# Performance work log

Hardware: AMD Instinct MI355X
Metric: run time of the kernel (lower is better)

## Reference

```python
import jax, jax.numpy as jnp
import numpy as np

N, E = 50000, 800000
IN_CH, OUT_CH, HEADS = 128, 64, 4
NEG_SLOPE = 0.2
BN_EPS = 1e-5


def setup_inputs() -> dict:
    key = jax.random.key(0)
    ks = jax.random.split(key, 8)
    x = jax.random.normal(ks[0], (N, IN_CH), dtype=jnp.float32)
    edge_index = jax.random.randint(ks[1], (2, E), 0, N, dtype=jnp.int64)
    # GATConv params (concat=False: W projects to H*C, output averaged over heads)
    W = jax.random.normal(ks[2], (IN_CH, HEADS * OUT_CH), dtype=jnp.float32) * (1.0 / np.sqrt(IN_CH))
    att_src = jax.random.normal(ks[3], (HEADS, OUT_CH), dtype=jnp.float32) * 0.1
    att_dst = jax.random.normal(ks[4], (HEADS, OUT_CH), dtype=jnp.float32) * 0.1
    bias = jnp.zeros((OUT_CH,), dtype=jnp.float32)
    bn_weight = jnp.ones((OUT_CH,), dtype=jnp.float32)
    bn_bias = jnp.zeros((OUT_CH,), dtype=jnp.float32)
    return {"x": x, "edge_index": edge_index, "W": W, "att_src": att_src,
            "att_dst": att_dst, "bias": bias, "bn_weight": bn_weight, "bn_bias": bn_bias}


def reference(x, edge_index, W, att_src, att_dst, bias, bn_weight, bn_bias):
    # dropout p=0.3 on input and attention weights: identity in eval mode
    n = x.shape[0]
    x_proj = (x @ W).reshape(n, HEADS, OUT_CH)              # [N, H, C]
    a_src = jnp.einsum('nhc,hc->nh', x_proj, att_src)       # [N, H]
    a_dst = jnp.einsum('nhc,hc->nh', x_proj, att_dst)       # [N, H]

    # PyG default add_self_loops=True
    loops = jnp.arange(n, dtype=edge_index.dtype)
    src = jnp.concatenate([edge_index[0], loops])           # [E+N]
    dst = jnp.concatenate([edge_index[1], loops])           # [E+N]

    e = jax.nn.leaky_relu(a_src[src] + a_dst[dst], NEG_SLOPE)  # [E+N, H]
    # edge-softmax per destination node (numerically stable)
    m = jax.ops.segment_max(e, dst, num_segments=n)         # [N, H]
    ex = jnp.exp(e - m[dst])
    denom = jax.ops.segment_sum(ex, dst, num_segments=n)    # [N, H]
    alpha = ex / denom[dst]                                 # [E+N, H]

    msg = alpha[:, :, None] * x_proj[src]                   # [E+N, H, C]
    out = jax.ops.segment_sum(msg, dst, num_segments=n)     # [N, H, C]
    out = out.mean(axis=1) + bias                           # concat=False -> head mean

    # BatchNorm (training-mode batch statistics, biased variance)
    mu = out.mean(axis=0)
    var = out.var(axis=0)
    out = (out - mu) * jax.lax.rsqrt(var + BN_EPS) * bn_weight + bn_bias
    return jax.nn.elu(out)
```

## Files before the change

kernel.cpp:

```cpp
#include <hip/hip_runtime.h>

#define IN_CH 128
#define HC 256
#define OUT_CH 64
#define NEG 0.2f
#define BN_EPS 1e-5f
#define APITCH 136
#define CSR_CAP 8192

typedef __attribute__((ext_vector_type(8))) short short8v;
typedef __attribute__((ext_vector_type(4))) float f32x4v;

__device__ __forceinline__ float4 add4(float4 a, float4 b) {
    return make_float4(a.x + b.x, a.y + b.y, a.z + b.z, a.w + b.w);
}
__device__ __forceinline__ float4 mul4(float4 a, float4 b) {
    return make_float4(a.x * b.x, a.y * b.y, a.z * b.z, a.w * b.w);
}
__device__ __forceinline__ float4 exp4f(float4 a) {
    return make_float4(__expf(a.x), __expf(a.y), __expf(a.z), __expf(a.w));
}
__device__ __forceinline__ float4 leaky4(float4 v) {
    v.x = v.x > 0.f ? v.x : v.x * NEG;
    v.y = v.y > 0.f ? v.y : v.y * NEG;
    v.z = v.z > 0.f ? v.z : v.z * NEG;
    v.w = v.w > 0.f ? v.w : v.w * NEG;
    return v;
}
__device__ __forceinline__ unsigned short f2bf(float f) {
    unsigned u = __float_as_uint(f);
    unsigned r = u + 0x7fffu + ((u >> 16) & 1u);
    return (unsigned short)(r >> 16);
}
__device__ __forceinline__ void acc8(float4& a, float ws, unsigned u) {
    a.x += ws * (float)(u & 0xffu);
    a.y += ws * (float)((u >> 8) & 0xffu);
    a.z += ws * (float)((u >> 16) & 0xffu);
    a.w += ws * (float)(u >> 24);
}

__global__ __launch_bounds__(256) void prep_wt(const float* __restrict__ W,
                                               unsigned short* __restrict__ wt,
                                               unsigned* __restrict__ zeros, int nz) {
    int idx = blockIdx.x * 256 + threadIdx.x;
    if (idx < nz) zeros[idx] = 0u;
    if (idx >= 64 * 64) return;
    int frag = idx >> 6, l = idx & 63;
    int j = frag >> 2, ks = frag & 3;
    int c = l & 15, g = l >> 4;
    int ch = c * 16 + j;
    int k0 = ks * 32 + g * 8;
    unsigned up[4];
    #pragma unroll
    for (int q = 0; q < 4; ++q) {
        unsigned short lo = f2bf(W[(size_t)(k0 + 2 * q) * HC + ch]);
        unsigned short hi = f2bf(W[(size_t)(k0 + 2 * q + 1) * HC + ch]);
        up[q] = (unsigned)lo | ((unsigned)hi << 16);
    }
    *(uint4*)(wt + (size_t)idx * 8) = make_uint4(up[0], up[1], up[2], up[3]);
}

__global__ __launch_bounds__(256) void gemm_mfma(const float* __restrict__ x,
                                                 const unsigned short* __restrict__ wt,
                                                 const float* __restrict__ att_src,
                                                 const float* __restrict__ att_dst,
                                                 unsigned char* __restrict__ xq,
                                                 float* __restrict__ pks,
                                                 float* __restrict__ adst, int N) {
    __shared__ unsigned short Al[64][APITCH];
    int t = threadIdx.x;
    int r0 = blockIdx.x * 64;
    #pragma unroll
    for (int i = 0; i < 8; ++i) {
        int f4 = t + i * 256;
        int m = f4 >> 5, kf = f4 & 31;
        float4 v = make_float4(0.f, 0.f, 0.f, 0.f);
        int r = r0 + m;
        if (r < N) v = *(const float4*)(x + (size_t)r * IN_CH + kf * 4);
        ushort4 pk;
        pk.x = f2bf(v.x); pk.y = f2bf(v.y); pk.z = f2bf(v.z); pk.w = f2bf(v.w);
        *(ushort4*)(&Al[m][kf * 4]) = pk;
    }
    __syncthreads();

    int w = t >> 6, l = t & 63;
    int c = l & 15, g = l >> 4;
    int arow = w * 16 + c;

    f32x4v acc[16];
    #pragma unroll
    for (int j = 0; j < 16; ++j) acc[j] = (f32x4v){0.f, 0.f, 0.f, 0.f};

    #pragma unroll
    for (int ks = 0; ks < 4; ++ks) {
        short8v a = *(const short8v*)(&Al[arow][ks * 32 + g * 8]);
        #pragma unroll
        for (int j = 0; j < 16; ++j) {
            short8v b = *(const short8v*)(wt + (size_t)((j * 4 + ks) * 64 + l) * 8);
            acc[j] = __builtin_amdgcn_mfma_f32_16x16x32_bf16(a, b, acc[j], 0, 0, 0);
        }
    }

    float as_c[16], ad_c[16];
    #pragma unroll
    for (int q = 0; q < 4; ++q) {
        *(float4*)(&as_c[q * 4]) = *(const float4*)(att_src + c * 16 + q * 4);
        *(float4*)(&ad_c[q * 4]) = *(const float4*)(att_dst + c * 16 + q * 4);
    }
    #pragma unroll
    for (int i = 0; i < 4; ++i) {
        int r = r0 + w * 16 + g * 4 + i;
        float ps = 0.f, pd = 0.f;
        float amax = 0.f;
        #pragma unroll
        for (int j = 0; j < 16; ++j) {
            float av = acc[j][i];
            ps += av * as_c[j];
            pd += av * ad_c[j];
            amax = fmaxf(amax, fabsf(av));
        }
        ps += __shfl_xor(ps, 1, 64); pd += __shfl_xor(pd, 1, 64);
        ps += __shfl_xor(ps, 2, 64); pd += __shfl_xor(pd, 2, 64);
        amax = fmaxf(amax, __shfl_xor(amax, 1, 64));
        amax = fmaxf(amax, __shfl_xor(amax, 2, 64));
        float inv = amax > 0.f ? 127.f / amax : 0.f;
        if (r < N) {
            int q4 = c & 3, h = c >> 2;
            if (q4 == 0) pks[(size_t)r * 8 + h] = ps;
            else if (q4 == 1) adst[(size_t)r * 4 + h] = pd;
            else if (q4 == 2) pks[(size_t)r * 8 + 4 + h] = amax * (1.f / 127.f);
            unsigned* orow = (unsigned*)(xq + (size_t)r * HC);
            #pragma unroll
            for (int q = 0; q < 4; ++q) {
                unsigned b0 = (unsigned)(int)fmaf(acc[q * 4 + 0][i], inv, 128.5f);
                unsigned b1 = (unsigned)(int)fmaf(acc[q * 4 + 1][i], inv, 128.5f);
                unsigned b2 = (unsigned)(int)fmaf(acc[q * 4 + 2][i], inv, 128.5f);
                unsigned b3 = (unsigned)(int)fmaf(acc[q * 4 + 3][i], inv, 128.5f);
                unsigned pk = b0 | (b1 << 8) | (b2 << 16) | (b3 << 24);
                orow[(((c & 3) * 4 + q) << 2) + h] = pk;
            }
        }
    }
}

__global__ __launch_bounds__(256) void bucket_scatter(const int* __restrict__ ei,
                                                      unsigned* __restrict__ bucket_cnt,
                                                      unsigned* __restrict__ bucketbuf,
                                                      int E) {
    __shared__ unsigned lcnt[256], lbase[256], lcur[256];
    int t = threadIdx.x;
    lcnt[t] = 0u; lcur[t] = 0u;
    __syncthreads();
    int c0 = blockIdx.x * 4096;
    unsigned rec[16];
    int bk[16];
    #pragma unroll
    for (int i = 0; i < 16; ++i) {
        int e = c0 + t + i * 256;
        bk[i] = -1;
        if (e < E) {
            unsigned s = (unsigned)ei[e];
            unsigned d = (unsigned)ei[E + e];
            rec[i] = s | ((d & 255u) << 16);
            bk[i] = (int)(d >> 8);
            atomicAdd(&lcnt[bk[i]], 1u);
        }
    }
    __syncthreads();
    lbase[t] = lcnt[t] ? atomicAdd(&bucket_cnt[t], lcnt[t]) : 0u;
    __syncthreads();
    #pragma unroll
    for (int i = 0; i < 16; ++i) {
        if (bk[i] >= 0) {
            unsigned p = lbase[bk[i]] + atomicAdd(&lcur[bk[i]], 1u);
            if (p < CSR_CAP) bucketbuf[(size_t)bk[i] * CSR_CAP + p] = rec[i];
        }
    }
}

__global__ __launch_bounds__(256) void bucket_csr(const unsigned* __restrict__ bucketbuf,
                                                  const unsigned* __restrict__ bucket_cnt,
                                                  unsigned* __restrict__ rowptr,
                                                  unsigned short* __restrict__ ssrc,
                                                  int N, int E, int NB) {
    __shared__ unsigned csum[256], dcnt[256], dscan[256], curo[256];
    __shared__ unsigned short sstage[CSR_CAP];
    int b = blockIdx.x, t = threadIdx.x;
    csum[t] = (t < NB) ? bucket_cnt[t] : 0u;
    dcnt[t] = 0u;
    __syncthreads();
    for (int o = 1; o < 256; o <<= 1) {
        unsigned v = (t >= o) ? csum[t - o] : 0u;
        __syncthreads();
        csum[t] += v;
        __syncthreads();
    }
    unsigned base = (b == 0) ? 0u : csum[b - 1];
    unsigned nloc = bucket_cnt[b];
    if (nloc > CSR_CAP) nloc = CSR_CAP;
    const unsigned* bb = bucketbuf + (size_t)b * CSR_CAP;
    for (unsigned i = t; i < nloc; i += 256) atomicAdd(&dcnt[bb[i] >> 16], 1u);
    __syncthreads();
    dscan[t] = dcnt[t];
    __syncthreads();
    for (int o = 1; o < 256; o <<= 1) {
        unsigned v = (t >= o) ? dscan[t - o] : 0u;
        __syncthreads();
        dscan[t] += v;
        __syncthreads();
    }
    unsigned loff = dscan[t] - dcnt[t];
    curo[t] = loff;
    int node = b * 256 + t;
    if (node < N) rowptr[node] = base + loff;
    if (b == 0 && t == 0) rowptr[N] = (unsigned)E;
    __syncthreads();
    for (unsigned i = t; i < nloc; i += 256) {
        unsigned r = bb[i];
        unsigned p = atomicAdd(&curo[r >> 16], 1u);
        sstage[p] = (unsigned short)(r & 0xffffu);
    }
    __syncthreads();
    for (unsigned i = t; i < nloc; i += 256) ssrc[base + i] = sstage[i];
}

__global__ __launch_bounds__(256) void node_fused(const unsigned short* __restrict__ ssrc,
                                                  const unsigned* __restrict__ rowptr,
                                                  const float* __restrict__ pks,
                                                  const float* __restrict__ adst,
                                                  const unsigned char* __restrict__ xq,
                                                  float* __restrict__ out, int N) {
    int wid = (blockIdx.x * 256 + threadIdx.x) >> 6;
    if (wid >= N) return;
    int lane = threadIdx.x & 63;
    int row0 = rowptr[wid];
    int deg = (int)rowptr[wid + 1] - row0;

    float4 ad = *(const float4*)(adst + (size_t)wid * 4);
    float4 saw = *(const float4*)(pks + (size_t)wid * 8);
    float4 scw = *(const float4*)(pks + (size_t)wid * 8 + 4);

    bool isEdge = lane < deg;
    bool active = lane <= deg;
    int s0 = wid;
    float4 as_s = saw, sc_s = scw;
    if (isEdge) {
        s0 = ssrc[row0 + lane];
        as_s = *(const float4*)(pks + (size_t)s0 * 8);
        sc_s = *(const float4*)(pks + (size_t)s0 * 8 + 4);
    }
    float4 ex0 = make_float4(0.f, 0.f, 0.f, 0.f);
    if (active) ex0 = exp4f(leaky4(add4(as_s, ad)));
    float4 sum = ex0;
    if (deg >= 64) {
        for (int j = lane + 64; j < deg; j += 64) {
            int s = ssrc[row0 + j];
            float4 lv = leaky4(add4(*(const float4*)(pks + (size_t)s * 8), ad));
            sum = add4(sum, exp4f(lv));
        }
        if (lane == 63) sum = add4(sum, exp4f(leaky4(add4(saw, ad))));
    }
    #pragma unroll
    for (int m = 1; m < 64; m <<= 1) {
        sum.x += __shfl_xor(sum.x, m, 64);
        sum.y += __shfl_xor(sum.y, m, 64);
        sum.z += __shfl_xor(sum.z, m, 64);
        sum.w += __shfl_xor(sum.w, m, 64);
    }
    float4 inv4 = make_float4(0.25f / sum.x, 0.25f / sum.y, 0.25f / sum.z, 0.25f / sum.w);
    float4 wsv = mul4(mul4(ex0, sc_s), inv4);

    int grp = lane >> 4, sub = lane & 15;
    float4 acc = make_float4(0.f, 0.f, 0.f, 0.f);
    float wssum = 0.f;

    if (deg < 64) {
        int nIter = (deg + 4) >> 2;
        #pragma unroll 2
        for (int it = 0; it < nIter; ++it) {
            int e = it * 4 + grp;
            int s = __shfl(s0, e, 64);
            float w0 = __shfl(wsv.x, e, 64), w1 = __shfl(wsv.y, e, 64);
            float w2 = __shfl(wsv.z, e, 64), w3 = __shfl(wsv.w, e, 64);
            uint4 u = *(const uint4*)(xq + (size_t)s * HC + sub * 16);
            acc8(acc, w0, u.x); acc8(acc, w1, u.y);
            acc8(acc, w2, u.z); acc8(acc, w3, u.w);
            wssum += w0 + w1 + w2 + w3;
        }
    } else {
        float4 selfws = mul4(mul4(exp4f(leaky4(add4(saw, ad))), scw), inv4);
        for (int jb = 0; jb <= deg; jb += 4) {
            int e = jb + grp;
            int ec = e < 64 ? e : 0;
            int s_sh = __shfl(s0, ec, 64);
            float w0 = __shfl(wsv.x, ec, 64), w1 = __shfl(wsv.y, ec, 64);
            float w2 = __shfl(wsv.z, ec, 64), w3 = __shfl(wsv.w, ec, 64);
            int s;
            float4 wv4;
            if (e < deg) {
                if (e < 64) {
                    s = s_sh;
                    wv4 = make_float4(w0, w1, w2, w3);
                } else {
                    s = ssrc[row0 + e];
                    float4 glv = leaky4(add4(*(const float4*)(pks + (size_t)s * 8), ad));
                    float4 gsc = *(const float4*)(pks + (size_t)s * 8 + 4);
                    wv4 = mul4(mul4(exp4f(glv), gsc), inv4);
                }
            } else if (e == deg) {
                s = wid; wv4 = selfws;
            } else {
                s = wid; wv4 = make_float4(0.f, 0.f, 0.f, 0.f);
            }
            uint4 u = *(const uint4*)(xq + (size_t)s * HC + sub * 16);
            acc8(acc, wv4.x, u.x); acc8(acc, wv4.y, u.y);
            acc8(acc, wv4.z, u.z); acc8(acc, wv4.w, u.w);
            wssum += wv4.x + wv4.y + wv4.z + wv4.w;
        }
    }

    #pragma unroll
    for (int m = 16; m < 64; m <<= 1) {
        acc.x += __shfl_xor(acc.x, m, 64);
        acc.y += __shfl_xor(acc.y, m, 64);
        acc.z += __shfl_xor(acc.z, m, 64);
        acc.w += __shfl_xor(acc.w, m, 64);
        wssum += __shfl_xor(wssum, m, 64);
    }
    float off = 128.f * wssum;
    if (lane < 16) {
        float4 o4 = make_float4(acc.x - off, acc.y - off, acc.z - off, acc.w - off);
        *(float4*)(out + (size_t)wid * OUT_CH + sub * 4) = o4;
    }
}

__global__ __launch_bounds__(256) void bn_stats(const float* __restrict__ out,
                                                float* __restrict__ sums,
                                                float* __restrict__ sqs, int N) {
    int c = threadIdx.x & 63, rl = threadIdx.x >> 6;
    float s = 0.f, q = 0.f;
    for (int r = blockIdx.x * 4 + rl; r < N; r += gridDim.x * 4) {
        float v = out[(size_t)r * 64 + c];
        s += v; q += v * v;
    }
    __shared__ float sb[256], qb[256];
    sb[threadIdx.x] = s; qb[threadIdx.x] = q;
    __syncthreads();
    if (rl == 0) {
        s = sb[c] + sb[64 + c] + sb[128 + c] + sb[192 + c];
        q = qb[c] + qb[64 + c] + qb[128 + c] + qb[192 + c];
        atomicAdd(sums + c, s);
        atomicAdd(sqs + c, q);
    }
}

__global__ __launch_bounds__(256) void finalize(float* __restrict__ out,
                                                const float* __restrict__ bnw,
                                                const float* __restrict__ bnb,
                                                const float* __restrict__ sums,
                                                const float* __restrict__ sqs, int N) {
    int idx = blockIdx.x * 256 + threadIdx.x;
    if (idx >= N * 64) return;
    int c = idx & 63;
    float invN = 1.0f / (float)N;
    float mu = sums[c] * invN;
    float var = sqs[c] * invN - mu * mu;
    float v = out[idx];
    float y = (v - mu) * rsqrtf(var + BN_EPS) * bnw[c] + bnb[c];
    out[idx] = y > 0.f ? y : expm1f(y);
}

extern "C" void kernel_launch(void* const* d_in, const int* in_sizes, int n_in,
                              void* d_out, int out_size, void* d_ws, size_t ws_size,
                              hipStream_t stream) {
    const float* x       = (const float*)d_in[0];
    const int*   ei      = (const int*)d_in[1];
    const float* W       = (const float*)d_in[2];
    const float* att_src = (const float*)d_in[3];
    const float* att_dst = (const float*)d_in[4];
    const float* bnw     = (const float*)d_in[6];
    const float* bnb     = (const float*)d_in[7];
    int N = in_sizes[0] / IN_CH;
    int E = in_sizes[1] / 2;
    float* out = (float*)d_out;
    int NB = (N + 255) / 256;

    unsigned char*  xq        = (unsigned char*)d_ws;
    unsigned short* wt        = (unsigned short*)(xq + (size_t)N * HC);
    float*          pks       = (float*)(wt + 64 * 64 * 8);
    float*          adst      = pks + (size_t)N * 8;
    unsigned*       bucket_cnt= (unsigned*)(adst + (size_t)N * 4);
    float*          sums      = (float*)(bucket_cnt + 256);
    float*          sqs       = sums + 64;
    unsigned*       rowptr    = (unsigned*)(sqs + 64);
    unsigned*       bucketbuf = rowptr + N + 1;
    unsigned short* ssrc      = (unsigned short*)(bucketbuf + (size_t)NB * CSR_CAP);

    prep_wt<<<16, 256, 0, stream>>>(W, wt, bucket_cnt, 384);
    gemm_mfma<<<(N + 63) / 64, 256, 0, stream>>>(x, wt, att_src, att_dst, xq, pks, adst, N);

    bucket_scatter<<<(E + 4095) / 4096, 256, 0, stream>>>(ei, bucket_cnt, bucketbuf, E);
    bucket_csr<<<NB, 256, 0, stream>>>(bucketbuf, bucket_cnt, rowptr, ssrc, N, E, NB);

    int gn = (N + 3) / 4;
    node_fused<<<gn, 256, 0, stream>>>(ssrc, rowptr, pks, adst, xq, out, N);

    bn_stats<<<1024, 256, 0, stream>>>(out, sums, sqs, N);
    finalize<<<((N * 64) + 255) / 256, 256, 0, stream>>>(out, bnw, bnb, sums, sqs, N);
}
```

Measured before the change: 131.4 us.

## Merge GEMM and edge bucket scatter into one launch; widen CSR build blocks

The projection GEMM and the edge bucket-scatter kernel are independent, so they now run as one launch whose block index picks the role. This removes one kernel launch and lets the scatter blocks run alongside the GEMM blocks. Separately, bucket_csr now uses 512 threads per block, with the scans guarded to the first 256 threads, so the per-bucket edge loops take half as many iterations. The combined kernel carries the shared memory of both roles, which may lower occupancy.

```diff
diff --git a/kernel.cpp b/kernel.cpp
--- a/kernel.cpp
+++ b/kernel.cpp
@@ -60,15 +60,52 @@
     *(uint4*)(wt + (size_t)idx * 8) = make_uint4(up[0], up[1], up[2], up[3]);
 }
 
-__global__ __launch_bounds__(256) void gemm_mfma(const float* __restrict__ x,
-                                                 const unsigned short* __restrict__ wt,
-                                                 const float* __restrict__ att_src,
-                                                 const float* __restrict__ att_dst,
-                                                 unsigned char* __restrict__ xq,
-                                                 float* __restrict__ pks,
-                                                 float* __restrict__ adst, int N) {
+__global__ __launch_bounds__(256) void gemm_and_scatter(const float* __restrict__ x,
+                                                        const unsigned short* __restrict__ wt,
+                                                        const float* __restrict__ att_src,
+                                                        const float* __restrict__ att_dst,
+                                                        unsigned char* __restrict__ xq,
+                                                        float* __restrict__ pks,
+                                                        float* __restrict__ adst, int N,
+                                                        const int* __restrict__ ei,
+                                                        unsigned* __restrict__ bucket_cnt,
+                                                        unsigned* __restrict__ bucketbuf,
+                                                        int E, int gemmBlocks) {
     __shared__ unsigned short Al[64][APITCH];
+    __shared__ unsigned lcnt[256], lbase[256], lcur[256];
     int t = threadIdx.x;
+
+    if ((int)blockIdx.x >= gemmBlocks) {
+        lcnt[t] = 0u; lcur[t] = 0u;
+        __syncthreads();
+        int c0 = ((int)blockIdx.x - gemmBlocks) * 4096;
+        unsigned rec[16];
+        int bk[16];
+        #pragma unroll
+        for (int i = 0; i < 16; ++i) {
+            int e = c0 + t + i * 256;
+            bk[i] = -1;
+            if (e < E) {
+                unsigned s = (unsigned)ei[e];
+                unsigned d = (unsigned)ei[E + e];
+                rec[i] = s | ((d & 255u) << 16);
+                bk[i] = (int)(d >> 8);
+                atomicAdd(&lcnt[bk[i]], 1u);
+            }
+        }
+        __syncthreads();
+        lbase[t] = lcnt[t] ? atomicAdd(&bucket_cnt[t], lcnt[t]) : 0u;
+        __syncthreads();
+        #pragma unroll
+        for (int i = 0; i < 16; ++i) {
+            if (bk[i] >= 0) {
+                unsigned p = lbase[bk[i]] + atomicAdd(&lcur[bk[i]], 1u);
+                if (p < CSR_CAP) bucketbuf[(size_t)bk[i] * CSR_CAP + p] = rec[i];
+            }
+        }
+        return;
+    }
+
     int r0 = blockIdx.x * 64;
     #pragma unroll
     for (int i = 0; i < 8; ++i) {
@@ -143,42 +180,7 @@
     }
 }
 
-__global__ __launch_bounds__(256) void bucket_scatter(const int* __restrict__ ei,
-                                                      unsigned* __restrict__ bucket_cnt,
-                                                      unsigned* __restrict__ bucketbuf,
-                                                      int E) {
-    __shared__ unsigned lcnt[256], lbase[256], lcur[256];
-    int t = threadIdx.x;
-    lcnt[t] = 0u; lcur[t] = 0u;
-    __syncthreads();
-    int c0 = blockIdx.x * 4096;
-    unsigned rec[16];
-    int bk[16];
-    #pragma unroll
-    for (int i = 0; i < 16; ++i) {
-        int e = c0 + t + i * 256;
-        bk[i] = -1;
-        if (e < E) {
-            unsigned s = (unsigned)ei[e];
-            unsigned d = (unsigned)ei[E + e];
-            rec[i] = s | ((d & 255u) << 16);
-            bk[i] = (int)(d >> 8);
-            atomicAdd(&lcnt[bk[i]], 1u);
-        }
-    }
-    __syncthreads();
-    lbase[t] = lcnt[t] ? atomicAdd(&bucket_cnt[t], lcnt[t]) : 0u;
-    __syncthreads();
-    #pragma unroll
-    for (int i = 0; i < 16; ++i) {
-        if (bk[i] >= 0) {
-            unsigned p = lbase[bk[i]] + atomicAdd(&lcur[bk[i]], 1u);
-            if (p < CSR_CAP) bucketbuf[(size_t)bk[i] * CSR_CAP + p] = rec[i];
-        }
-    }
-}
-
-__global__ __launch_bounds__(256) void bucket_csr(const unsigned* __restrict__ bucketbuf,
+__global__ __launch_bounds__(512) void bucket_csr(const unsigned* __restrict__ bucketbuf,
                                                   const unsigned* __restrict__ bucket_cnt,
                                                   unsigned* __restrict__ rowptr,
                                                   unsigned short* __restrict__ ssrc,
@@ -186,42 +188,48 @@
     __shared__ unsigned csum[256], dcnt[256], dscan[256], curo[256];
     __shared__ unsigned short sstage[CSR_CAP];
     int b = blockIdx.x, t = threadIdx.x;
-    csum[t] = (t < NB) ? bucket_cnt[t] : 0u;
-    dcnt[t] = 0u;
+    if (t < 256) {
+        csum[t] = (t < NB) ? bucket_cnt[t] : 0u;
+        dcnt[t] = 0u;
+    }
     __syncthreads();
     for (int o = 1; o < 256; o <<= 1) {
-        unsigned v = (t >= o) ? csum[t - o] : 0u;
-        __syncthreads();
-        csum[t] += v;
+        unsigned v = 0u;
+        if (t < 256 && t >= o) v = csum[t - o];
+        __syncthreads();
+        if (t < 256) csum[t] += v;
         __syncthreads();
     }
     unsigned base = (b == 0) ? 0u : csum[b - 1];
     unsigned nloc = bucket_cnt[b];
     if (nloc > CSR_CAP) nloc = CSR_CAP;
     const unsigned* bb = bucketbuf + (size_t)b * CSR_CAP;
-    for (unsigned i = t; i < nloc; i += 256) atomicAdd(&dcnt[bb[i] >> 16], 1u);
-    __syncthreads();
-    dscan[t] = dcnt[t];
+    for (unsigned i = t; i < nloc; i += 512) atomicAdd(&dcnt[bb[i] >> 16], 1u);
+    __syncthreads();
+    if (t < 256) dscan[t] = dcnt[t];
     __syncthreads();
     for (int o = 1; o < 256; o <<= 1) {
-        unsigned v = (t >= o) ? dscan[t - o] : 0u;
-        __syncthreads();
-        dscan[t] += v;
-        __syncthreads();
-    }
-    unsigned loff = dscan[t] - dcnt[t];
-    curo[t] = loff;
-    int node = b * 256 + t;
-    if (node < N) rowptr[node] = base + loff;
+        unsigned v = 0u;
+        if (t < 256 && t >= o) v = dscan[t - o];
+        __syncthreads();
+        if (t < 256) dscan[t] += v;
+        __syncthreads();
+    }
+    if (t < 256) {
+        unsigned loff = dscan[t] - dcnt[t];
+        curo[t] = loff;
+        int node = b * 256 + t;
+        if (node < N) rowptr[node] = base + loff;
+    }
     if (b == 0 && t == 0) rowptr[N] = (unsigned)E;
     __syncthreads();
-    for (unsigned i = t; i < nloc; i += 256) {
+    for (unsigned i = t; i < nloc; i += 512) {
         unsigned r = bb[i];
         unsigned p = atomicAdd(&curo[r >> 16], 1u);
         sstage[p] = (unsigned short)(r & 0xffffu);
     }
     __syncthreads();
-    for (unsigned i = t; i < nloc; i += 256) ssrc[base + i] = sstage[i];
+    for (unsigned i = t; i < nloc; i += 512) ssrc[base + i] = sstage[i];
 }
 
 __global__ __launch_bounds__(256) void node_fused(const unsigned short* __restrict__ ssrc,
@@ -397,10 +405,13 @@
     unsigned short* ssrc      = (unsigned short*)(bucketbuf + (size_t)NB * CSR_CAP);
 
     prep_wt<<<16, 256, 0, stream>>>(W, wt, bucket_cnt, 384);
-    gemm_mfma<<<(N + 63) / 64, 256, 0, stream>>>(x, wt, att_src, att_dst, xq, pks, adst, N);
-
-    bucket_scatter<<<(E + 4095) / 4096, 256, 0, stream>>>(ei, bucket_cnt, bucketbuf, E);
-    bucket_csr<<<NB, 256, 0, stream>>>(bucketbuf, bucket_cnt, rowptr, ssrc, N, E, NB);
+
+    int gemmBlocks = (N + 63) / 64;
+    int scatBlocks = (E + 4095) / 4096;
+    gemm_and_scatter<<<gemmBlocks + scatBlocks, 256, 0, stream>>>(
+        x, wt, att_src, att_dst, xq, pks, adst, N, ei, bucket_cnt, bucketbuf, E, gemmBlocks);
+
+    bucket_csr<<<NB, 512, 0, stream>>>(bucketbuf, bucket_cnt, rowptr, ssrc, N, E, NB);
 
     int gn = (N + 3) / 4;
     node_fused<<<gn, 256, 0, stream>>>(ssrc, rowptr, pks, adst, xq, out, N);
```

New measurement: 120.7 us. 1.09x faster.
